# Kernel optimization log

Hardware: AMD Instinct MI355X
Metric: run time of the kernel (lower is better)

## Reference

```python
import jax, jax.numpy as jnp
import numpy as np

N_NODES = 200000
N_BONDS = 220000
D = 128


def setup_inputs() -> dict:
    key = jax.random.key(0)
    ks = jax.random.split(key, 8)
    h = jax.random.normal(ks[0], (N_NODES, D), dtype=jnp.float32)
    src = jax.random.randint(ks[1], (N_BONDS,), 0, N_NODES, dtype=jnp.int64)
    dst = jax.random.randint(ks[2], (N_BONDS,), 0, N_NODES, dtype=jnp.int64)
    # MLP params (Sequential: Linear(256,128)+ReLU, Linear(128,128)+ReLU, Linear(128,2))
    W1 = jax.random.normal(ks[3], (2 * D, 128), dtype=jnp.float32) * (1.0 / np.sqrt(2 * D))
    b1 = jnp.zeros((128,), dtype=jnp.float32)
    W2 = jax.random.normal(ks[4], (128, 128), dtype=jnp.float32) * (1.0 / np.sqrt(128))
    b2 = jnp.zeros((128,), dtype=jnp.float32)
    W3 = jax.random.normal(ks[5], (128, 2), dtype=jnp.float32) * (1.0 / np.sqrt(128))
    b3 = jnp.zeros((2,), dtype=jnp.float32)
    return {"h": h, "src": src, "dst": dst,
            "W1": W1, "b1": b1, "W2": W2, "b2": b2, "W3": W3, "b3": b3}


def _mlp(x, W1, b1, W2, b2, W3, b3):
    x = jax.nn.relu(x @ W1 + b1)
    x = jax.nn.relu(x @ W2 + b2)
    return x @ W3 + b3


def reference(h, src, dst, W1, b1, W2, b2, W3, b3):
    # forward edges: (src -> dst); reverse edges: (dst -> src)
    h_src = h[src]            # [E, D] gather
    h_dst = h[dst]            # [E, D] gather
    h_forward = jnp.concatenate([h_src, h_dst], axis=1)  # [E, 2D]
    h_reverse = jnp.concatenate([h_dst, h_src], axis=1)  # [E, 2D]
    return (_mlp(h_forward, W1, b1, W2, b2, W3, b3)
            + _mlp(h_reverse, W1, b1, W2, b2, W3, b3))
```

## Files before the change

kernel.cpp:

```cpp
#include <hip/hip_runtime.h>
#include <hip/hip_bf16.h>
#include <stdint.h>


typedef __attribute__((ext_vector_type(8))) short bf16x8;
typedef __attribute__((ext_vector_type(4))) float f32x4;

__device__ __forceinline__ float bf2f(unsigned u16) {
    union { unsigned u; float f; } v; v.u = u16 << 16;
    return v.f;
}
__device__ __forceinline__ unsigned short f2bf(float f) {
    union { float f; unsigned u; } v; v.f = f;
    unsigned u = v.u;
    unsigned r = u + 0x7FFFu + ((u >> 16) & 1u);
    return (unsigned short)(r >> 16);
}

__device__ __forceinline__ int swz(int f, int c) {
    return f * 128 + ((c ^ (f & 7)) << 3);
}
__device__ __forceinline__ int swzA(int f, int c) {
    return f * 256 + ((c ^ (f & 7)) << 3);
}

__device__ __forceinline__ bf16x8 cvt8v(float4 x, float4 y) {
    union { bf16x8 v; __hip_bfloat162 h[4]; } R;
    R.h[0] = __float22bfloat162_rn(float2{x.x, x.y});
    R.h[1] = __float22bfloat162_rn(float2{x.z, x.w});
    R.h[2] = __float22bfloat162_rn(float2{y.x, y.y});
    R.h[3] = __float22bfloat162_rn(float2{y.z, y.w});
    return R.v;
}

#define MFMA(a, b, c) __builtin_amdgcn_mfma_f32_16x16x32_bf16((a), (b), (c), 0, 0, 0)

__global__ void prep_weights(const float* __restrict__ W1,
                             const float* __restrict__ W2,
                             unsigned short* __restrict__ W1c,
                             unsigned short* __restrict__ W2t) {
    int idx = blockIdx.x * 256 + threadIdx.x;
    if (idx < 128 * 256) {
        int j = idx >> 8, k = idx & 255;
        W1c[idx] = f2bf(W1[k * 128 + j]);
    } else {
        int i2 = idx - 128 * 256;
        if (i2 < 128 * 128) {
            int n = i2 >> 7, k = i2 & 127;
            W2t[i2] = f2bf(W2[k * 128 + n]);
        }
    }
}

__global__ __launch_bounds__(512, 1) void edge_fused(
    const float* __restrict__ h, const int* __restrict__ src,
    const int* __restrict__ dst, const unsigned short* __restrict__ W1c,
    const unsigned short* __restrict__ W2t, const float* __restrict__ b1,
    const float* __restrict__ b2, const float* __restrict__ W3,
    const float* __restrict__ b3, float* __restrict__ out, int E) {
    __shared__ unsigned short W1s[128 * 256];
    __shared__ unsigned short W2s[128 * 128];
    __shared__ unsigned short scr[8 * 16 * 128];
    __shared__ float  cb1[128];
    __shared__ float  cb2[128];
    __shared__ float2 cW3[128];

    int t = threadIdx.x;
    int lane = t & 63;
    int wv = t >> 6;
    int ml = lane & 15, quad = lane >> 4;

    {
        int r = t >> 2, q = t & 3;
        const uint4* s = (const uint4*)(W1c + (size_t)r * 256 + q * 64);
#pragma unroll
        for (int i = 0; i < 8; ++i)
            *(uint4*)(W1s + swzA(r, q * 8 + i)) = s[i];
    }
    {
        int f = t >> 2, q4 = t & 3;
        const uint4* s = (const uint4*)(W2t + (size_t)f * 128 + q4 * 32);
#pragma unroll
        for (int i = 0; i < 4; ++i)
            *(uint4*)(W2s + swz(f, q4 * 4 + i)) = s[i];
    }
    if (t < 128) {
        cb1[t] = b1[t];
        cb2[t] = b2[t];
        cW3[t] = float2{W3[t * 2 + 0], W3[t * 2 + 1]};
    }

    int e = blockIdx.x * 128 + wv * 16 + ml;
    int ec = (e < E) ? e : (E - 1);
    int si = src[ec], di = dst[ec];
    const float* hs = h + (size_t)si * 128;
    const float* hd = h + (size_t)di * 128;

    float4 s0a, s0b, s1a, s1b, s2a, s2b, s3a, s3b;
    float4 d0a, d0b, d1a, d1b, d2a, d2b, d3a, d3b;
    {
        int ko = quad * 8;
        s0a = *(const float4*)(hs + ko);       s0b = *(const float4*)(hs + ko + 4);
        s1a = *(const float4*)(hs + 32 + ko);  s1b = *(const float4*)(hs + 36 + ko);
        s2a = *(const float4*)(hs + 64 + ko);  s2b = *(const float4*)(hs + 68 + ko);
        s3a = *(const float4*)(hs + 96 + ko);  s3b = *(const float4*)(hs + 100 + ko);
        d0a = *(const float4*)(hd + ko);       d0b = *(const float4*)(hd + ko + 4);
        d1a = *(const float4*)(hd + 32 + ko);  d1b = *(const float4*)(hd + 36 + ko);
        d2a = *(const float4*)(hd + 64 + ko);  d2b = *(const float4*)(hd + 68 + ko);
        d3a = *(const float4*)(hd + 96 + ko);  d3b = *(const float4*)(hd + 100 + ko);
    }
    bf16x8 hsf[4], hdf[4];
    hsf[0] = cvt8v(s0a, s0b); hsf[1] = cvt8v(s1a, s1b);
    hsf[2] = cvt8v(s2a, s2b); hsf[3] = cvt8v(s3a, s3b);
    hdf[0] = cvt8v(d0a, d0b); hdf[1] = cvt8v(d1a, d1b);
    hdf[2] = cvt8v(d2a, d2b); hdf[3] = cvt8v(d3a, d3b);

    __syncthreads();

    unsigned short* scrW = scr + wv * 2048;
    bf16x8 afw[4], arv[4];

    {
        f32x4 accf[8] = {}, accr[8] = {};
        __builtin_amdgcn_s_setprio(1);
#pragma unroll
        for (int kk = 0; kk < 4; ++kk) {
#pragma unroll
            for (int ct = 0; ct < 8; ++ct) {
                bf16x8 a = *(const bf16x8*)(W1s + swzA(ct * 16 + ml, kk * 4 + quad));
                accf[ct] = MFMA(a, hsf[kk], accf[ct]);
                accr[ct] = MFMA(a, hdf[kk], accr[ct]);
            }
        }
#pragma unroll
        for (int kk = 4; kk < 8; ++kk) {
#pragma unroll
            for (int ct = 0; ct < 8; ++ct) {
                bf16x8 a = *(const bf16x8*)(W1s + swzA(ct * 16 + ml, kk * 4 + quad));
                accf[ct] = MFMA(a, hdf[kk - 4], accf[ct]);
                accr[ct] = MFMA(a, hsf[kk - 4], accr[ct]);
            }
        }
        __builtin_amdgcn_s_setprio(0);

#pragma unroll
        for (int ct = 0; ct < 8; ++ct) {
            int fb = ct * 16 + quad * 4;
            float4 bv = *(const float4*)(cb1 + fb);
            union { uint2 u; __hip_bfloat162 h2[2]; } o;
            o.h2[0] = __float22bfloat162_rn(float2{fmaxf(accf[ct][0] + bv.x, 0.f),
                                                   fmaxf(accf[ct][1] + bv.y, 0.f)});
            o.h2[1] = __float22bfloat162_rn(float2{fmaxf(accf[ct][2] + bv.z, 0.f),
                                                   fmaxf(accf[ct][3] + bv.w, 0.f)});
            int chunk = ct * 2 + (quad >> 1);
            *(uint2*)(scrW + ml * 128 + ((chunk ^ (ml & 7)) << 3) + ((quad & 1) << 2)) = o.u;
        }
        __threadfence_block();
#pragma unroll
        for (int kk = 0; kk < 4; ++kk) {
            int chunk = kk * 4 + quad;
            afw[kk] = *(const bf16x8*)(scrW + ml * 128 + ((chunk ^ (ml & 7)) << 3));
        }
        __threadfence_block();

#pragma unroll
        for (int ct = 0; ct < 8; ++ct) {
            int fb = ct * 16 + quad * 4;
            float4 bv = *(const float4*)(cb1 + fb);
            union { uint2 u; __hip_bfloat162 h2[2]; } o;
            o.h2[0] = __float22bfloat162_rn(float2{fmaxf(accr[ct][0] + bv.x, 0.f),
                                                   fmaxf(accr[ct][1] + bv.y, 0.f)});
            o.h2[1] = __float22bfloat162_rn(float2{fmaxf(accr[ct][2] + bv.z, 0.f),
                                                   fmaxf(accr[ct][3] + bv.w, 0.f)});
            int chunk = ct * 2 + (quad >> 1);
            *(uint2*)(scrW + ml * 128 + ((chunk ^ (ml & 7)) << 3) + ((quad & 1) << 2)) = o.u;
        }
        __threadfence_block();
#pragma unroll
        for (int kk = 0; kk < 4; ++kk) {
            int chunk = kk * 4 + quad;
            arv[kk] = *(const bf16x8*)(scrW + ml * 128 + ((chunk ^ (ml & 7)) << 3));
        }
    }

    float p0[4] = {0.f, 0.f, 0.f, 0.f};
    float p1[4] = {0.f, 0.f, 0.f, 0.f};
    {
        f32x4 acc2f[8] = {}, acc2r[8] = {};
        __builtin_amdgcn_s_setprio(1);
#pragma unroll
        for (int kk = 0; kk < 4; ++kk) {
#pragma unroll
            for (int ct = 0; ct < 8; ++ct) {
                bf16x8 b = *(const bf16x8*)(W2s + swz(ct * 16 + ml, kk * 4 + quad));
                acc2f[ct] = MFMA(afw[kk], b, acc2f[ct]);
                acc2r[ct] = MFMA(arv[kk], b, acc2r[ct]);
            }
        }
        __builtin_amdgcn_s_setprio(0);
#pragma unroll
        for (int ct = 0; ct < 8; ++ct) {
            int c = ct * 16 + ml;
            float2 w3 = cW3[c];
            float bc = cb2[c];
#pragma unroll
            for (int reg = 0; reg < 4; ++reg) {
                float hf = fmaxf(acc2f[ct][reg] + bc, 0.f);
                float hr = fmaxf(acc2r[ct][reg] + bc, 0.f);
                p0[reg] += (hf + hr) * w3.x;
                p1[reg] += (hf + hr) * w3.y;
            }
        }
    }

#pragma unroll
    for (int m = 1; m < 16; m <<= 1) {
#pragma unroll
        for (int reg = 0; reg < 4; ++reg) {
            p0[reg] += __shfl_xor(p0[reg], m);
            p1[reg] += __shfl_xor(p1[reg], m);
        }
    }

    if (ml < 2) {
        float bb = 2.f * b3[ml];
#pragma unroll
        for (int reg = 0; reg < 4; ++reg) {
            int ee = blockIdx.x * 128 + wv * 16 + quad * 4 + reg;
            if (ee < E) {
                float v = (ml == 0) ? p0[reg] : p1[reg];
                out[(size_t)ee * 2 + ml] = v + bb;
            }
        }
    }
}

extern "C" void kernel_launch(void* const* d_in, const int* in_sizes, int n_in,
                              void* d_out, int out_size, void* d_ws, size_t ws_size,
                              hipStream_t stream) {
    (void)n_in; (void)out_size; (void)ws_size;
    const float* h  = (const float*)d_in[0];
    const int*   sr = (const int*)d_in[1];
    const int*   ds = (const int*)d_in[2];
    const float* W1 = (const float*)d_in[3];
    const float* b1 = (const float*)d_in[4];
    const float* W2 = (const float*)d_in[5];
    const float* b2 = (const float*)d_in[6];
    const float* W3 = (const float*)d_in[7];
    const float* b3 = (const float*)d_in[8];
    float* out = (float*)d_out;

    int E = in_sizes[1];

    unsigned short* W1c = (unsigned short*)d_ws;
    unsigned short* W2t = W1c + 128 * 256;

    prep_weights<<<(128 * 256 + 128 * 128 + 255) / 256, 256, 0, stream>>>(W1, W2, W1c, W2t);

    int etiles = (E + 127) / 128;
    edge_fused<<<etiles, 512, 0, stream>>>(h, sr, ds, W1c, W2t, b1, b2, W3, b3, out, E);
}
```

Measured before the change: 228.2 us.

## Process two edge tiles per block to amortize shared-memory weight staging

Each block now handles 256 edges as two 128-edge tiles. It gathers both tiles' node features up front, then runs the MLP body, factored into a helper, once per tile. This halves the number of times W1/W2 are copied from global memory into LDS per edge and overlaps the second tile's gather latency with the first tile's compute. Launch bounds change to ask for two blocks per CU, which limits per-thread registers and may cause spills. The LDS footprint of about 128KB per block probably still allows only one resident block.

Measured after the change: 228.5 us. Within noise of the previous version (+0.1%).

```diff
diff --git a/kernel.cpp b/kernel.cpp
--- a/kernel.cpp
+++ b/kernel.cpp
@@ -52,7 +52,131 @@
     }
 }
 
-__global__ __launch_bounds__(512, 1) void edge_fused(
+__device__ __forceinline__ void mlp_tile(
+    const unsigned short* W1s, const unsigned short* W2s,
+    unsigned short* scrW, const float* cb1, const float* cb2,
+    const float2* cW3, const float* __restrict__ b3,
+    const bf16x8* hsf, const bf16x8* hdf,
+    int ml, int quad, int ebase, float* __restrict__ out, int E) {
+    bf16x8 afw[4], arv[4];
+
+    {
+        f32x4 accf[8] = {}, accr[8] = {};
+        __builtin_amdgcn_s_setprio(1);
+#pragma unroll
+        for (int kk = 0; kk < 4; ++kk) {
+#pragma unroll
+            for (int ct = 0; ct < 8; ++ct) {
+                bf16x8 a = *(const bf16x8*)(W1s + swzA(ct * 16 + ml, kk * 4 + quad));
+                accf[ct] = MFMA(a, hsf[kk], accf[ct]);
+                accr[ct] = MFMA(a, hdf[kk], accr[ct]);
+            }
+        }
+#pragma unroll
+        for (int kk = 4; kk < 8; ++kk) {
+#pragma unroll
+            for (int ct = 0; ct < 8; ++ct) {
+                bf16x8 a = *(const bf16x8*)(W1s + swzA(ct * 16 + ml, kk * 4 + quad));
+                accf[ct] = MFMA(a, hdf[kk - 4], accf[ct]);
+                accr[ct] = MFMA(a, hsf[kk - 4], accr[ct]);
+            }
+        }
+        __builtin_amdgcn_s_setprio(0);
+
+#pragma unroll
+        for (int ct = 0; ct < 8; ++ct) {
+            int fb = ct * 16 + quad * 4;
+            float4 bv = *(const float4*)(cb1 + fb);
+            union { uint2 u; __hip_bfloat162 h2[2]; } o;
+            o.h2[0] = __float22bfloat162_rn(float2{fmaxf(accf[ct][0] + bv.x, 0.f),
+                                                   fmaxf(accf[ct][1] + bv.y, 0.f)});
+            o.h2[1] = __float22bfloat162_rn(float2{fmaxf(accf[ct][2] + bv.z, 0.f),
+                                                   fmaxf(accf[ct][3] + bv.w, 0.f)});
+            int chunk = ct * 2 + (quad >> 1);
+            *(uint2*)(scrW + ml * 128 + ((chunk ^ (ml & 7)) << 3) + ((quad & 1) << 2)) = o.u;
+        }
+        __threadfence_block();
+#pragma unroll
+        for (int kk = 0; kk < 4; ++kk) {
+            int chunk = kk * 4 + quad;
+            afw[kk] = *(const bf16x8*)(scrW + ml * 128 + ((chunk ^ (ml & 7)) << 3));
+        }
+        __threadfence_block();
+
+#pragma unroll
+        for (int ct = 0; ct < 8; ++ct) {
+            int fb = ct * 16 + quad * 4;
+            float4 bv = *(const float4*)(cb1 + fb);
+            union { uint2 u; __hip_bfloat162 h2[2]; } o;
+            o.h2[0] = __float22bfloat162_rn(float2{fmaxf(accr[ct][0] + bv.x, 0.f),
+                                                   fmaxf(accr[ct][1] + bv.y, 0.f)});
+            o.h2[1] = __float22bfloat162_rn(float2{fmaxf(accr[ct][2] + bv.z, 0.f),
+                                                   fmaxf(accr[ct][3] + bv.w, 0.f)});
+            int chunk = ct * 2 + (quad >> 1);
+            *(uint2*)(scrW + ml * 128 + ((chunk ^ (ml & 7)) << 3) + ((quad & 1) << 2)) = o.u;
+        }
+        __threadfence_block();
+#pragma unroll
+        for (int kk = 0; kk < 4; ++kk) {
+            int chunk = kk * 4 + quad;
+            arv[kk] = *(const bf16x8*)(scrW + ml * 128 + ((chunk ^ (ml & 7)) << 3));
+        }
+        __threadfence_block();
+    }
+
+    float p0[4] = {0.f, 0.f, 0.f, 0.f};
+    float p1[4] = {0.f, 0.f, 0.f, 0.f};
+    {
+        f32x4 acc2f[8] = {}, acc2r[8] = {};
+        __builtin_amdgcn_s_setprio(1);
+#pragma unroll
+        for (int kk = 0; kk < 4; ++kk) {
+#pragma unroll
+            for (int ct = 0; ct < 8; ++ct) {
+                bf16x8 b = *(const bf16x8*)(W2s + swz(ct * 16 + ml, kk * 4 + quad));
+                acc2f[ct] = MFMA(afw[kk], b, acc2f[ct]);
+                acc2r[ct] = MFMA(arv[kk], b, acc2r[ct]);
+            }
+        }
+        __builtin_amdgcn_s_setprio(0);
+#pragma unroll
+        for (int ct = 0; ct < 8; ++ct) {
+            int c = ct * 16 + ml;
+            float2 w3 = cW3[c];
+            float bc = cb2[c];
+#pragma unroll
+            for (int reg = 0; reg < 4; ++reg) {
+                float hf = fmaxf(acc2f[ct][reg] + bc, 0.f);
+                float hr = fmaxf(acc2r[ct][reg] + bc, 0.f);
+                p0[reg] += (hf + hr) * w3.x;
+                p1[reg] += (hf + hr) * w3.y;
+            }
+        }
+    }
+
+#pragma unroll
+    for (int m = 1; m < 16; m <<= 1) {
+#pragma unroll
+        for (int reg = 0; reg < 4; ++reg) {
+            p0[reg] += __shfl_xor(p0[reg], m);
+            p1[reg] += __shfl_xor(p1[reg], m);
+        }
+    }
+
+    if (ml < 2) {
+        float bb = 2.f * b3[ml];
+#pragma unroll
+        for (int reg = 0; reg < 4; ++reg) {
+            int ee = ebase + quad * 4 + reg;
+            if (ee < E) {
+                float v = (ml == 0) ? p0[reg] : p1[reg];
+                out[(size_t)ee * 2 + ml] = v + bb;
+            }
+        }
+    }
+}
+
+__global__ __launch_bounds__(512, 2) void edge_fused(
     const float* __restrict__ h, const int* __restrict__ src,
     const int* __restrict__ dst, const unsigned short* __restrict__ W1c,
     const unsigned short* __restrict__ W2t, const float* __restrict__ b1,
@@ -90,149 +214,53 @@
         cW3[t] = float2{W3[t * 2 + 0], W3[t * 2 + 1]};
     }
 
-    int e = blockIdx.x * 128 + wv * 16 + ml;
-    int ec = (e < E) ? e : (E - 1);
-    int si = src[ec], di = dst[ec];
-    const float* hs = h + (size_t)si * 128;
-    const float* hd = h + (size_t)di * 128;
-
-    float4 s0a, s0b, s1a, s1b, s2a, s2b, s3a, s3b;
-    float4 d0a, d0b, d1a, d1b, d2a, d2b, d3a, d3b;
-    {
-        int ko = quad * 8;
-        s0a = *(const float4*)(hs + ko);       s0b = *(const float4*)(hs + ko + 4);
-        s1a = *(const float4*)(hs + 32 + ko);  s1b = *(const float4*)(hs + 36 + ko);
-        s2a = *(const float4*)(hs + 64 + ko);  s2b = *(const float4*)(hs + 68 + ko);
-        s3a = *(const float4*)(hs + 96 + ko);  s3b = *(const float4*)(hs + 100 + ko);
-        d0a = *(const float4*)(hd + ko);       d0b = *(const float4*)(hd + ko + 4);
-        d1a = *(const float4*)(hd + 32 + ko);  d1b = *(const float4*)(hd + 36 + ko);
-        d2a = *(const float4*)(hd + 64 + ko);  d2b = *(const float4*)(hd + 68 + ko);
-        d3a = *(const float4*)(hd + 96 + ko);  d3b = *(const float4*)(hd + 100 + ko);
-    }
-    bf16x8 hsf[4], hdf[4];
-    hsf[0] = cvt8v(s0a, s0b); hsf[1] = cvt8v(s1a, s1b);
-    hsf[2] = cvt8v(s2a, s2b); hsf[3] = cvt8v(s3a, s3b);
-    hdf[0] = cvt8v(d0a, d0b); hdf[1] = cvt8v(d1a, d1b);
-    hdf[2] = cvt8v(d2a, d2b); hdf[3] = cvt8v(d3a, d3b);
+    int eA = blockIdx.x * 256 + wv * 16 + ml;
+    int eB = eA + 128;
+    int ecA = (eA < E) ? eA : (E - 1);
+    int ecB = (eB < E) ? eB : (E - 1);
+    int siA = src[ecA], diA = dst[ecA];
+    int siB = src[ecB], diB = dst[ecB];
+    const float* hsA = h + (size_t)siA * 128;
+    const float* hdA = h + (size_t)diA * 128;
+    const float* hsB = h + (size_t)siB * 128;
+    const float* hdB = h + (size_t)diB * 128;
+    int ko = quad * 8;
+
+    float4 As0a = *(const float4*)(hsA + ko);       float4 As0b = *(const float4*)(hsA + ko + 4);
+    float4 As1a = *(const float4*)(hsA + 32 + ko);  float4 As1b = *(const float4*)(hsA + 36 + ko);
+    float4 As2a = *(const float4*)(hsA + 64 + ko);  float4 As2b = *(const float4*)(hsA + 68 + ko);
+    float4 As3a = *(const float4*)(hsA + 96 + ko);  float4 As3b = *(const float4*)(hsA + 100 + ko);
+    float4 Ad0a = *(const float4*)(hdA + ko);       float4 Ad0b = *(const float4*)(hdA + ko + 4);
+    float4 Ad1a = *(const float4*)(hdA + 32 + ko);  float4 Ad1b = *(const float4*)(hdA + 36 + ko);
+    float4 Ad2a = *(const float4*)(hdA + 64 + ko);  float4 Ad2b = *(const float4*)(hdA + 68 + ko);
+    float4 Ad3a = *(const float4*)(hdA + 96 + ko);  float4 Ad3b = *(const float4*)(hdA + 100 + ko);
+    float4 Bs0a = *(const float4*)(hsB + ko);       float4 Bs0b = *(const float4*)(hsB + ko + 4);
+    float4 Bs1a = *(const float4*)(hsB + 32 + ko);  float4 Bs1b = *(const float4*)(hsB + 36 + ko);
+    float4 Bs2a = *(const float4*)(hsB + 64 + ko);  float4 Bs2b = *(const float4*)(hsB + 68 + ko);
+    float4 Bs3a = *(const float4*)(hsB + 96 + ko);  float4 Bs3b = *(const float4*)(hsB + 100 + ko);
+    float4 Bd0a = *(const float4*)(hdB + ko);       float4 Bd0b = *(const float4*)(hdB + ko + 4);
+    float4 Bd1a = *(const float4*)(hdB + 32 + ko);  float4 Bd1b = *(const float4*)(hdB + 36 + ko);
+    float4 Bd2a = *(const float4*)(hdB + 64 + ko);  float4 Bd2b = *(const float4*)(hdB + 68 + ko);
+    float4 Bd3a = *(const float4*)(hdB + 96 + ko);  float4 Bd3b = *(const float4*)(hdB + 100 + ko);
+
+    bf16x8 hsfA[4], hdfA[4], hsfB[4], hdfB[4];
+    hsfA[0] = cvt8v(As0a, As0b); hsfA[1] = cvt8v(As1a, As1b);
+    hsfA[2] = cvt8v(As2a, As2b); hsfA[3] = cvt8v(As3a, As3b);
+    hdfA[0] = cvt8v(Ad0a, Ad0b); hdfA[1] = cvt8v(Ad1a, Ad1b);
+    hdfA[2] = cvt8v(Ad2a, Ad2b); hdfA[3] = cvt8v(Ad3a, Ad3b);
+    hsfB[0] = cvt8v(Bs0a, Bs0b); hsfB[1] = cvt8v(Bs1a, Bs1b);
+    hsfB[2] = cvt8v(Bs2a, Bs2b); hsfB[3] = cvt8v(Bs3a, Bs3b);
+    hdfB[0] = cvt8v(Bd0a, Bd0b); hdfB[1] = cvt8v(Bd1a, Bd1b);
+    hdfB[2] = cvt8v(Bd2a, Bd2b); hdfB[3] = cvt8v(Bd3a, Bd3b);
 
     __syncthreads();
 
     unsigned short* scrW = scr + wv * 2048;
-    bf16x8 afw[4], arv[4];
-
-    {
-        f32x4 accf[8] = {}, accr[8] = {};
-        __builtin_amdgcn_s_setprio(1);
-#pragma unroll
-        for (int kk = 0; kk < 4; ++kk) {
-#pragma unroll
-            for (int ct = 0; ct < 8; ++ct) {
-                bf16x8 a = *(const bf16x8*)(W1s + swzA(ct * 16 + ml, kk * 4 + quad));
-                accf[ct] = MFMA(a, hsf[kk], accf[ct]);
-                accr[ct] = MFMA(a, hdf[kk], accr[ct]);
-            }
-        }
-#pragma unroll
-        for (int kk = 4; kk < 8; ++kk) {
-#pragma unroll
-            for (int ct = 0; ct < 8; ++ct) {
-                bf16x8 a = *(const bf16x8*)(W1s + swzA(ct * 16 + ml, kk * 4 + quad));
-                accf[ct] = MFMA(a, hdf[kk - 4], accf[ct]);
-                accr[ct] = MFMA(a, hsf[kk - 4], accr[ct]);
-            }
-        }
-        __builtin_amdgcn_s_setprio(0);
-
-#pragma unroll
-        for (int ct = 0; ct < 8; ++ct) {
-            int fb = ct * 16 + quad * 4;
-            float4 bv = *(const float4*)(cb1 + fb);
-            union { uint2 u; __hip_bfloat162 h2[2]; } o;
-            o.h2[0] = __float22bfloat162_rn(float2{fmaxf(accf[ct][0] + bv.x, 0.f),
-                                                   fmaxf(accf[ct][1] + bv.y, 0.f)});
-            o.h2[1] = __float22bfloat162_rn(float2{fmaxf(accf[ct][2] + bv.z, 0.f),
-                                                   fmaxf(accf[ct][3] + bv.w, 0.f)});
-            int chunk = ct * 2 + (quad >> 1);
-            *(uint2*)(scrW + ml * 128 + ((chunk ^ (ml & 7)) << 3) + ((quad & 1) << 2)) = o.u;
-        }
-        __threadfence_block();
-#pragma unroll
-        for (int kk = 0; kk < 4; ++kk) {
-            int chunk = kk * 4 + quad;
-            afw[kk] = *(const bf16x8*)(scrW + ml * 128 + ((chunk ^ (ml & 7)) << 3));
-        }
-        __threadfence_block();
-
-#pragma unroll
-        for (int ct = 0; ct < 8; ++ct) {
-            int fb = ct * 16 + quad * 4;
-            float4 bv = *(const float4*)(cb1 + fb);
-            union { uint2 u; __hip_bfloat162 h2[2]; } o;
-            o.h2[0] = __float22bfloat162_rn(float2{fmaxf(accr[ct][0] + bv.x, 0.f),
-                                                   fmaxf(accr[ct][1] + bv.y, 0.f)});
-            o.h2[1] = __float22bfloat162_rn(float2{fmaxf(accr[ct][2] + bv.z, 0.f),
-                                                   fmaxf(accr[ct][3] + bv.w, 0.f)});
-            int chunk = ct * 2 + (quad >> 1);
-            *(uint2*)(scrW + ml * 128 + ((chunk ^ (ml & 7)) << 3) + ((quad & 1) << 2)) = o.u;
-        }
-        __threadfence_block();
-#pragma unroll
-        for (int kk = 0; kk < 4; ++kk) {
-            int chunk = kk * 4 + quad;
-            arv[kk] = *(const bf16x8*)(scrW + ml * 128 + ((chunk ^ (ml & 7)) << 3));
-        }
-    }
-
-    float p0[4] = {0.f, 0.f, 0.f, 0.f};
-    float p1[4] = {0.f, 0.f, 0.f, 0.f};
-    {
-        f32x4 acc2f[8] = {}, acc2r[8] = {};
-        __builtin_amdgcn_s_setprio(1);
-#pragma unroll
-        for (int kk = 0; kk < 4; ++kk) {
-#pragma unroll
-            for (int ct = 0; ct < 8; ++ct) {
-                bf16x8 b = *(const bf16x8*)(W2s + swz(ct * 16 + ml, kk * 4 + quad));
-                acc2f[ct] = MFMA(afw[kk], b, acc2f[ct]);
-                acc2r[ct] = MFMA(arv[kk], b, acc2r[ct]);
-            }
-        }
-        __builtin_amdgcn_s_setprio(0);
-#pragma unroll
-        for (int ct = 0; ct < 8; ++ct) {
-            int c = ct * 16 + ml;
-            float2 w3 = cW3[c];
-            float bc = cb2[c];
-#pragma unroll
-            for (int reg = 0; reg < 4; ++reg) {
-                float hf = fmaxf(acc2f[ct][reg] + bc, 0.f);
-                float hr = fmaxf(acc2r[ct][reg] + bc, 0.f);
-                p0[reg] += (hf + hr) * w3.x;
-                p1[reg] += (hf + hr) * w3.y;
-            }
-        }
-    }
-
-#pragma unroll
-    for (int m = 1; m < 16; m <<= 1) {
-#pragma unroll
-        for (int reg = 0; reg < 4; ++reg) {
-            p0[reg] += __shfl_xor(p0[reg], m);
-            p1[reg] += __shfl_xor(p1[reg], m);
-        }
-    }
-
-    if (ml < 2) {
-        float bb = 2.f * b3[ml];
-#pragma unroll
-        for (int reg = 0; reg < 4; ++reg) {
-            int ee = blockIdx.x * 128 + wv * 16 + quad * 4 + reg;
-            if (ee < E) {
-                float v = (ml == 0) ? p0[reg] : p1[reg];
-                out[(size_t)ee * 2 + ml] = v + bb;
-            }
-        }
-    }
+
+    mlp_tile(W1s, W2s, scrW, cb1, cb2, cW3, b3, hsfA, hdfA,
+             ml, quad, blockIdx.x * 256 + wv * 16, out, E);
+    mlp_tile(W1s, W2s, scrW, cb1, cb2, cW3, b3, hsfB, hdfB,
+             ml, quad, blockIdx.x * 256 + 128 + wv * 16, out, E);
 }
 
 extern "C" void kernel_launch(void* const* d_in, const int* in_sizes, int n_in,
@@ -257,6 +285,6 @@
 
     prep_weights<<<(128 * 256 + 128 * 128 + 255) / 256, 256, 0, stream>>>(W1, W2, W1c, W2t);
 
-    int etiles = (E + 127) / 128;
+    int etiles = (E + 255) / 256;
     edge_fused<<<etiles, 512, 0, stream>>>(h, sr, ds, W1c, W2t, b1, b2, W3, b3, out, E);
 }
```
